# Performance work log

Hardware: AMD Instinct MI355X
Metric: run time of the kernel (lower is better)

Reference implementation:

```python
import jax, jax.numpy as jnp
import numpy as np

CODEBOOK_NUM = 4
VECTOR_NUM = 1024
VECTOR_DIM = 256
COMMIT_W = 0.25
N = 65536


def setup_inputs() -> dict:
    key = jax.random.key(0)
    kx, kw = jax.random.split(key)
    x = jax.random.normal(kx, (N, VECTOR_DIM), dtype=jnp.float32)
    # nn.Embedding init: uniform(-1/vector_num, 1/vector_num), one table per residual level
    codebooks = jax.random.uniform(
        kw, (CODEBOOK_NUM, VECTOR_NUM, VECTOR_DIM), dtype=jnp.float32,
        minval=-1.0 / VECTOR_NUM, maxval=1.0 / VECTOR_NUM)
    return {"x": x, "codebooks": codebooks}


def _pdist_mean(W):
    # mean of pairwise euclidean distances over i<j pairs (torch.pdist semantics)
    K = W.shape[0]
    sq = jnp.sum(W * W, axis=1)
    d2 = sq[:, None] + sq[None, :] - 2.0 * (W @ W.T)  # [K, K]
    mask = jnp.triu(jnp.ones((K, K), dtype=bool), k=1)
    d = jnp.sqrt(jnp.where(mask, jnp.maximum(d2, 0.0), 1.0))
    n_pairs = K * (K - 1) // 2
    return jnp.sum(jnp.where(mask, d, 0.0)) / n_pairs


def _vq_layer(residual, W):
    # distances [N, K]: ||r||^2 + ||w||^2 - 2 r.w
    dist = (jnp.sum(residual * residual, axis=1, keepdims=True)
            + jnp.sum(W * W, axis=1)
            - 2.0 * (residual @ W.T))
    idx = jnp.argmin(dist, axis=1)                    # [N]
    q = jnp.take(W, idx, axis=0)                      # gather == one_hot @ W (same value & grad)
    sg = jax.lax.stop_gradient
    e_latent = jnp.mean((sg(q) - residual) ** 2)
    q_latent = jnp.mean((q - sg(residual)) ** 2)
    quant_loss = q_latent + COMMIT_W * e_latent
    q_st = residual + sg(q - residual)                # straight-through
    counts = jnp.bincount(idx, length=W.shape[0]).astype(jnp.float32)
    util_loss = jnp.mean(jnp.abs(counts - residual.shape[0] / W.shape[0]))
    compact_loss = 2.0 * _pdist_mean(W)
    return q_st, quant_loss, util_loss, compact_loss, idx


def reference(x, codebooks):
    quantized = jnp.zeros_like(x)
    residual = x
    quant = jnp.float32(0.0)
    util = jnp.float32(0.0)
    compact = jnp.float32(0.0)
    all_idx = []
    for c in range(codebooks.shape[0]):
        q_st, ql, ul, cl, idx = _vq_layer(residual, codebooks[c])
        quantized = quantized + q_st
        residual = x - quantized
        quant = quant + ql
        util = util + ul
        compact = compact + cl
        all_idx.append(idx)
    return quantized, quant, util, compact, jnp.stack(all_idx, axis=0)
```

## Files before the change

kernel.cpp:

```cpp
#include <hip/hip_runtime.h>
#include <math.h>
#include <float.h>


#define N_ROWS 65536
#define DIM    256
#define K_NUM  1024
#define N_CB   4
#define RPB    32
#define QOFF   16777216
#define IDXOFF 16777219
#define NPAIRS 523776
#define MARGIN 2.4e-4f

#define SWZV(row, dunit) ((row) * DIM + ((((dunit) ^ ((row) & 7))) << 1))
#define SWZ2(row, d)     ((row) * DIM + ((((((d) >> 1) ^ ((row) & 7))) << 1) | ((d) & 1)))
#define AFCH(mt, kk, q, m) \
  (((((mt) * 8 + (kk)) * 64) + (q) * 16 + (((m) ^ ((q) << 1) ^ (kk)) & 15)) * 8)

typedef _Float16 f16x8 __attribute__((ext_vector_type(8)));
typedef float    f32x4 __attribute__((ext_vector_type(4)));

#define WS_BWS_OFF 69632
#define WS_NEEDED  2166784

__device__ __forceinline__ bool lexless(float a, int ka, float b, int kb) {
  return (a < b) || (a == b && ka < kb);
}

__global__ void zero_ws(int* counts, double* sse, double* pdacc) {
  int t = blockIdx.x * blockDim.x + threadIdx.x;
  if (t < 4096) counts[t] = 0;
  if (t < 4) sse[t] = 0.0;
  if (t == 0) pdacc[0] = 0.0;
}

__global__ void np_sqw_kernel(const float* __restrict__ cb,
                              float* __restrict__ sqw) {
#pragma clang fp contract(off)
  int g = blockIdx.x * blockDim.x + threadIdx.x;
  const float* row = cb + (size_t)g * DIM;
  float blk[2];
#pragma unroll
  for (int b = 0; b < 2; ++b) {
    const float* a = row + b * 128;
    float r[8];
#pragma unroll
    for (int j = 0; j < 8; ++j) { float v = a[j]; r[j] = v * v; }
    for (int i = 8; i < 128; i += 8) {
#pragma unroll
      for (int j = 0; j < 8; ++j) { float v = a[i + j]; r[j] = r[j] + v * v; }
    }
    blk[b] = ((r[0] + r[1]) + (r[2] + r[3])) + ((r[4] + r[5]) + (r[6] + r[7]));
  }
  sqw[g] = blk[0] + blk[1];
}

__global__ void cvt_b_kernel(const float* __restrict__ cb,
                             _Float16* __restrict__ bws) {
  int tg = blockIdx.x * blockDim.x + threadIdx.x;
  int row = tg >> 5;
  int chunk = tg & 31;
  int c = row >> 10, n = row & 1023;
  int nt = n >> 4, nin = n & 15;
  int kk = chunk >> 2, quad = chunk & 3;
  const float* src = cb + (size_t)row * DIM + chunk * 8;
  f16x8 h;
#pragma unroll
  for (int j = 0; j < 8; ++j) h[j] = (_Float16)src[j];
  size_t dst = ((size_t)((c * 64 + nt) * 8 + kk) * 64 + quad * 16 + nin) * 8;
  *(f16x8*)(bws + dst) = h;
}

__global__ __launch_bounds__(256) void pdist_mfma(
    const _Float16* __restrict__ bws, const float* __restrict__ sqw,
    double* __restrict__ pdacc) {
  int t = threadIdx.x, lane = t & 63, wq = t >> 6;
  int quad = lane >> 4, col = lane & 15;
  int c = blockIdx.x >> 6, iT = blockIdx.x & 63;
  const float* sq = sqw + c * K_NUM;
  const _Float16* base = bws + ((size_t)(c * 64) * 8) * 512 + lane * 8;
  f16x8 Ar[8];
#pragma unroll
  for (int kk = 0; kk < 8; ++kk)
    Ar[kk] = *(const f16x8*)(base + (size_t)(iT * 8 + kk) * 512);
  float bi[4];
#pragma unroll
  for (int r = 0; r < 4; ++r) bi[r] = sq[iT * 16 + quad * 4 + r];
  float sum = 0.f;
#pragma unroll 1
  for (int jt0 = 0; jt0 < 16; ++jt0) {
    int jt = wq * 16 + jt0;
    f16x8 Br[8];
#pragma unroll
    for (int kk = 0; kk < 8; ++kk)
      Br[kk] = *(const f16x8*)(base + (size_t)(jt * 8 + kk) * 512);
    f32x4 acc = {0.f, 0.f, 0.f, 0.f};
#pragma unroll
    for (int kk = 0; kk < 8; ++kk)
      acc = __builtin_amdgcn_mfma_f32_16x16x32_f16(Ar[kk], Br[kk], acc, 0, 0, 0);
    int j = jt * 16 + col;
    float bj = sq[j];
#pragma unroll
    for (int r = 0; r < 4; ++r) {
      int i = iT * 16 + quad * 4 + r;
      float d2 = bi[r] + bj - 2.0f * acc[r];
      if (i != j) sum += sqrtf(fmaxf(d2, 0.f));
    }
  }
  double ds = (double)sum;
#pragma unroll
  for (int off = 32; off; off >>= 1) ds += __shfl_xor(ds, off, 64);
  if (lane == 0) atomicAdd(pdacc, ds);
}

__global__ __launch_bounds__(256, 3) void rvq_main_mfma(
    const float* __restrict__ x, const float* __restrict__ cb,
    const _Float16* __restrict__ bws, const float* __restrict__ sqw,
    int* __restrict__ counts, double* __restrict__ sse,
    float* __restrict__ out) {
  __shared__ float resS[RPB * DIM];
  __shared__ __align__(16) _Float16 Af[16 * 64 * 8];
  __shared__ float wminS[RPB * 4];
  __shared__ int hardCnt[RPB];
  __shared__ int hardIdx[RPB * 6];
  __shared__ int idxS[RPB];
  __shared__ float sqrS[RPB];

  int t = threadIdx.x;
  int lane = t & 63, wq = t >> 6;
  int quad = lane >> 4, m16 = lane & 15;
  int rb = blockIdx.x * RPB;
  int dchunk = t & 31, rowgrp = t >> 5;

  float qacc[4][8];

#pragma unroll
  for (int i = 0; i < 4; ++i) {
    int row = rowgrp * 4 + i;
    size_t go = (size_t)(rb + row) * DIM + dchunk * 8;
    f32x4 v0 = __builtin_nontemporal_load((const f32x4*)&x[go]);
    f32x4 v1 = __builtin_nontemporal_load((const f32x4*)&x[go + 4]);
    float xv[8];
#pragma unroll
    for (int j = 0; j < 4; ++j) { xv[j] = v0[j]; xv[4 + j] = v1[j]; }
    f16x8 h;
#pragma unroll
    for (int j = 0; j < 8; ++j) h[j] = (_Float16)xv[j];
    *(f16x8*)(Af + AFCH(row >> 4, dchunk >> 2, dchunk & 3, row & 15)) = h;
    int u0 = dchunk * 4;
    *(float2*)&resS[SWZV(row, u0 + 0)] = make_float2(xv[0], xv[1]);
    *(float2*)&resS[SWZV(row, u0 + 1)] = make_float2(xv[2], xv[3]);
    *(float2*)&resS[SWZV(row, u0 + 2)] = make_float2(xv[4], xv[5]);
    *(float2*)&resS[SWZV(row, u0 + 3)] = make_float2(xv[6], xv[7]);
  }
  __syncthreads();

  for (int c = 0; c < N_CB; ++c) {
    const float* cbl = cb + (size_t)c * K_NUM * DIM;
    const float* sqwl = sqw + c * K_NUM;

    {
#pragma clang fp contract(off)
      int kg = t & 7, rg = t >> 3;
      float blk[2];
#pragma unroll
      for (int b = 0; b < 2; ++b) {
        float v0 = resS[SWZ2(rg, b * 128 + kg)];
        float acc = v0 * v0;
        for (int i = 1; i < 16; ++i) {
          float v = resS[SWZ2(rg, b * 128 + kg + 8 * i)];
          acc = acc + v * v;
        }
        acc = acc + __shfl_xor(acc, 1, 8);
        acc = acc + __shfl_xor(acc, 2, 8);
        acc = acc + __shfl_xor(acc, 4, 8);
        blk[b] = acc;
      }
      if (kg == 0) sqrS[rg] = blk[0] + blk[1];
    }

    f16x8 Ar[2][8];
#pragma unroll
    for (int kk = 0; kk < 8; ++kk) {
      Ar[0][kk] = *(const f16x8*)(Af + AFCH(0, kk, quad, m16));
      Ar[1][kk] = *(const f16x8*)(Af + AFCH(1, kk, quad, m16));
    }
    float s1[2][4], s2[2][4]; int k1[2][4], k2[2][4];
#pragma unroll
    for (int mt = 0; mt < 2; ++mt)
#pragma unroll
      for (int r = 0; r < 4; ++r) {
        s1[mt][r] = FLT_MAX; s2[mt][r] = FLT_MAX;
        k1[mt][r] = 0x7FFFFFFF; k2[mt][r] = 0x7FFFFFFF;
      }
    const _Float16* Bc = bws + (size_t)((c * 64 + wq * 16) * 8) * 512 + lane * 8;
#pragma unroll 1
    for (int nt = 0; nt < 16; ++nt) {
      const _Float16* Bp = Bc + (size_t)nt * 8 * 512;
      f16x8 Br[8];
#pragma unroll
      for (int kk = 0; kk < 8; ++kk)
        Br[kk] = *(const f16x8*)(Bp + (size_t)kk * 512);
      f32x4 acc0 = {0.f, 0.f, 0.f, 0.f}, acc1 = {0.f, 0.f, 0.f, 0.f};
#pragma unroll
      for (int kk = 0; kk < 8; ++kk) {
        acc0 = __builtin_amdgcn_mfma_f32_16x16x32_f16(Ar[0][kk], Br[kk], acc0, 0, 0, 0);
        acc1 = __builtin_amdgcn_mfma_f32_16x16x32_f16(Ar[1][kk], Br[kk], acc1, 0, 0, 0);
      }
      int n = (wq * 16 + nt) * 16 + m16;
      float w2 = sqwl[n];
#pragma unroll
      for (int r = 0; r < 4; ++r) {
        float sa = w2 - 2.0f * acc0[r];
        if (sa < s1[0][r]) { s2[0][r] = s1[0][r]; k2[0][r] = k1[0][r]; s1[0][r] = sa; k1[0][r] = n; }
        else if (sa < s2[0][r]) { s2[0][r] = sa; k2[0][r] = n; }
        float sb = w2 - 2.0f * acc1[r];
        if (sb < s1[1][r]) { s2[1][r] = s1[1][r]; k2[1][r] = k1[1][r]; s1[1][r] = sb; k1[1][r] = n; }
        else if (sb < s2[1][r]) { s2[1][r] = sb; k2[1][r] = n; }
      }
    }

    if (t < RPB) hardCnt[t] = 0;
#pragma unroll
    for (int mt = 0; mt < 2; ++mt)
#pragma unroll
      for (int r = 0; r < 4; ++r) {
        float mn = s1[mt][r];
#pragma unroll
        for (int off = 1; off <= 8; off <<= 1)
          mn = fminf(mn, __shfl_xor(mn, off, 16));
        if (m16 == 0) wminS[(mt * 16 + quad * 4 + r) * 4 + wq] = mn;
      }
    __syncthreads();

#pragma unroll
    for (int mt = 0; mt < 2; ++mt)
#pragma unroll
      for (int r = 0; r < 4; ++r) {
        int row = mt * 16 + quad * 4 + r;
        float thr = fminf(fminf(wminS[row * 4 + 0], wminS[row * 4 + 1]),
                          fminf(wminS[row * 4 + 2], wminS[row * 4 + 3])) + MARGIN;
        bool c1 = s1[mt][r] <= thr;
        if (c1) {
          bool c2 = s2[mt][r] <= thr;
          int pos = atomicAdd(&hardCnt[row], 1 + (c2 ? 1 : 0));
          if (pos < 6) hardIdx[row * 6 + pos] = k1[mt][r];
          if (c2 && pos + 1 < 6) hardIdx[row * 6 + pos + 1] = k2[mt][r];
        }
      }
    __syncthreads();

    {
      int kg = t & 7, rg = t >> 3;
      int cnt = hardCnt[rg]; if (cnt > 6) cnt = 6;
      int winner;
      if (cnt == 1) {
        winner = hardIdx[rg * 6];
      } else {
        float myd = FLT_MAX; int myk = 0x7FFFFFFF;
        if (kg < cnt) {
          int k = hardIdx[rg * 6 + kg];
          const float* wrow = cbl + (size_t)k * DIM;
          float gsum = 0.0f;
#pragma unroll 8
          for (int d = 0; d < DIM; ++d)
            gsum = __builtin_fmaf(wrow[d], resS[SWZ2(rg, d)], gsum);
          float T = sqrS[rg] + sqwl[k];
          myd = T - 2.0f * gsum;
          myk = k;
        }
#pragma unroll
        for (int off = 1; off <= 4; off <<= 1) {
          float od = __shfl_xor(myd, off, 8);
          int   ok = __shfl_xor(myk, off, 8);
          if (lexless(od, ok, myd, myk)) { myd = od; myk = ok; }
        }
        winner = myk;
      }
      if (kg == 0) {
        idxS[rg] = winner;
        out[(size_t)IDXOFF + (size_t)c * N_ROWS + rb + rg] = (float)winner;
        atomicAdd(&counts[c * K_NUM + winner], 1);
      }
    }
    __syncthreads();

    double lsse = 0.0;
#pragma unroll
    for (int i = 0; i < 4; ++i) {
      int row = rowgrp * 4 + i;
      int widx = idxS[row];
      size_t go = (size_t)(rb + row) * DIM + dchunk * 8;
      float wv[8], rv[8], xv[8];
      const float* wrow = cbl + (size_t)widx * DIM + dchunk * 8;
      *(float4*)&wv[0] = *(const float4*)&wrow[0];
      *(float4*)&wv[4] = *(const float4*)&wrow[4];
      int u0 = dchunk * 4;
      *(float2*)&rv[0] = *(const float2*)&resS[SWZV(row, u0 + 0)];
      *(float2*)&rv[2] = *(const float2*)&resS[SWZV(row, u0 + 1)];
      *(float2*)&rv[4] = *(const float2*)&resS[SWZV(row, u0 + 2)];
      *(float2*)&rv[6] = *(const float2*)&resS[SWZV(row, u0 + 3)];
      if (c == 1 || c == 2) {
        f32x4 xa = __builtin_nontemporal_load((const f32x4*)&x[go]);
        f32x4 xb = __builtin_nontemporal_load((const f32x4*)&x[go + 4]);
#pragma unroll
        for (int j = 0; j < 4; ++j) { xv[j] = xa[j]; xv[4 + j] = xb[j]; }
      }
      f16x8 h;
      float rnv[8];
#pragma unroll
      for (int j = 0; j < 8; ++j) {
        float e = wv[j] - rv[j];
        float qs = rv[j] + e;
        float qn = (c == 0) ? qs : (qacc[i][j] + qs);
        qacc[i][j] = qn;
        lsse += (double)e * (double)e;
        if (c < N_CB - 1) {
          float rn = (c == 0) ? (rv[j] - qn) : (xv[j] - qn);
          rnv[j] = rn;
          h[j] = (_Float16)rn;
        }
      }
      if (c < N_CB - 1) {
        *(f16x8*)(Af + AFCH(row >> 4, dchunk >> 2, dchunk & 3, row & 15)) = h;
        *(float2*)&resS[SWZV(row, u0 + 0)] = make_float2(rnv[0], rnv[1]);
        *(float2*)&resS[SWZV(row, u0 + 1)] = make_float2(rnv[2], rnv[3]);
        *(float2*)&resS[SWZV(row, u0 + 2)] = make_float2(rnv[4], rnv[5]);
        *(float2*)&resS[SWZV(row, u0 + 3)] = make_float2(rnv[6], rnv[7]);
      } else {
        f32x4 o0, o1;
#pragma unroll
        for (int j = 0; j < 4; ++j) { o0[j] = qacc[i][j]; o1[j] = qacc[i][4 + j]; }
        __builtin_nontemporal_store(o0, (f32x4*)&out[go]);
        __builtin_nontemporal_store(o1, (f32x4*)&out[go + 4]);
      }
    }
#pragma unroll
    for (int off = 32; off; off >>= 1) lsse += __shfl_xor(lsse, off, 64);
    if ((t & 63) == 0) atomicAdd(&sse[c], lsse);
    __syncthreads();
  }
}

__global__ void wnorm_kernel(const float* __restrict__ cb,
                             double* __restrict__ wn64) {
  int gw = blockIdx.x * 4 + (threadIdx.x >> 6);
  int lane = threadIdx.x & 63;
  const float* row = cb + (size_t)gw * DIM;
  float4 v = *(const float4*)(row + lane * 4);
  double s = (double)v.x * v.x + (double)v.y * v.y +
             (double)v.z * v.z + (double)v.w * v.w;
#pragma unroll
  for (int off = 32; off; off >>= 1) s += __shfl_xor(s, off, 64);
  if (lane == 0) wn64[gw] = s;
}

__global__ void pdist_kernel(const float* __restrict__ cb,
                             const double* __restrict__ wn64,
                             double* __restrict__ pdacc) {
  __shared__ float wi[DIM];
  int c = blockIdx.x >> 10;
  int i = blockIdx.x & 1023;
  int t = threadIdx.x;
  const float* rowi = cb + ((size_t)c * K_NUM + i) * DIM;
  *(float2*)&wi[t * 2] = *(const float2*)&rowi[t * 2];
  __syncthreads();
  double bi = wn64[c * K_NUM + i];
  double lsum = 0.0;
  for (int j = i + 1 + t; j < K_NUM; j += 128) {
    const float* rowj = cb + ((size_t)c * K_NUM + j) * DIM;
    double dot = 0.0;
#pragma unroll 8
    for (int d = 0; d < DIM; ++d) dot += (double)rowj[d] * (double)wi[d];
    double d2 = bi + wn64[c * K_NUM + j] - 2.0 * dot;
    lsum += sqrt(fmax(d2, 0.0));
  }
#pragma unroll
  for (int off = 32; off; off >>= 1) lsum += __shfl_xor(lsum, off, 64);
  if ((t & 63) == 0) atomicAdd(pdacc, lsum);
}

__global__ __launch_bounds__(128) void rvq_main_fb(
    const float* __restrict__ x, const float* __restrict__ cb,
    const float* __restrict__ sqw,
    int* __restrict__ counts, double* __restrict__ sse,
    float* __restrict__ out) {
  __shared__ float Wt[RPB * DIM];
  __shared__ float resS[RPB * DIM];
  int t = threadIdx.x;
  int kg = t & 7;
  int rg = t >> 3;
  int rb = blockIdx.x * RPB;
#pragma unroll 4
  for (int it = 0; it < RPB; ++it) {
    float2 v = *(const float2*)&x[(size_t)(rb + it) * DIM + t * 2];
    *(float2*)&resS[SWZV(it, t)] = v;
  }
  __syncthreads();
  for (int c = 0; c < N_CB; ++c) {
    const float* cbl = cb + (size_t)c * K_NUM * DIM;
    const float* sqwl = sqw + c * K_NUM;
    float sqr[2];
    {
#pragma clang fp contract(off)
#pragma unroll
      for (int j = 0; j < 2; ++j) {
        int row = rg + 16 * j;
        float blk[2];
#pragma unroll
        for (int b = 0; b < 2; ++b) {
          float v0 = resS[SWZ2(row, b * 128 + kg)];
          float acc = v0 * v0;
          for (int i = 1; i < 16; ++i) {
            float v = resS[SWZ2(row, b * 128 + kg + 8 * i)];
            acc = acc + v * v;
          }
          acc = acc + __shfl_xor(acc, 1, 8);
          acc = acc + __shfl_xor(acc, 2, 8);
          acc = acc + __shfl_xor(acc, 4, 8);
          blk[b] = acc;
        }
        sqr[j] = blk[0] + blk[1];
      }
    }
    float m1[2], m2[2]; int i1[2], i2[2];
    m1[0] = m1[1] = m2[0] = m2[1] = FLT_MAX;
    i1[0] = i1[1] = i2[0] = i2[1] = 0x7FFFFFFF;
    for (int tile = 0; tile < K_NUM / 32; ++tile) {
      __syncthreads();
      const float* wsrc = cbl + (size_t)tile * 32 * DIM;
#pragma unroll 4
      for (int it = 0; it < 32; ++it) {
        float2 v = *(const float2*)&wsrc[(size_t)it * DIM + t * 2];
        *(float2*)&Wt[SWZV(it, t)] = v;
      }
      __syncthreads();
      float acc[4][2] = {{0.f, 0.f}, {0.f, 0.f}, {0.f, 0.f}, {0.f, 0.f}};
#pragma unroll 8
      for (int du = 0; du < DIM / 2; ++du) {
        float2 r0 = *(const float2*)&resS[SWZV(rg, du)];
        float2 r1 = *(const float2*)&resS[SWZV(rg + 16, du)];
#pragma unroll
        for (int i = 0; i < 4; ++i) {
          int k = kg + 8 * i;
          float2 w = *(const float2*)&Wt[SWZV(k, du)];
          acc[i][0] += w.x * r0.x; acc[i][0] += w.y * r0.y;
          acc[i][1] += w.x * r1.x; acc[i][1] += w.y * r1.y;
        }
      }
#pragma unroll
      for (int i = 0; i < 4; ++i) {
        int k = tile * 32 + kg + 8 * i;
        float b = sqwl[k];
#pragma unroll
        for (int j = 0; j < 2; ++j) {
          float s = b - 2.0f * acc[i][j];
          if (lexless(s, k, m1[j], i1[j])) {
            m2[j] = m1[j]; i2[j] = i1[j]; m1[j] = s; i1[j] = k;
          } else if (lexless(s, k, m2[j], i2[j])) {
            m2[j] = s; i2[j] = k;
          }
        }
      }
    }
    float as[2][4]; int ak[2][4];
#pragma unroll
    for (int j = 0; j < 2; ++j) {
      as[j][0] = m1[j]; ak[j][0] = i1[j];
      as[j][1] = m2[j]; ak[j][1] = i2[j];
      as[j][2] = FLT_MAX; ak[j][2] = 0x7FFFFFFF;
      as[j][3] = FLT_MAX; ak[j][3] = 0x7FFFFFFF;
#pragma unroll
      for (int off = 1; off <= 4; off <<= 1) {
        float bs[4]; int bk[4];
#pragma unroll
        for (int q = 0; q < 4; ++q) {
          bs[q] = __shfl_xor(as[j][q], off, 8);
          bk[q] = __shfl_xor(ak[j][q], off, 8);
        }
        float cs[4]; int ck[4];
#pragma unroll
        for (int q = 0; q < 4; ++q) {
          bool ta = lexless(as[j][q], ak[j][q], bs[3 - q], bk[3 - q]);
          cs[q] = ta ? as[j][q] : bs[3 - q];
          ck[q] = ta ? ak[j][q] : bk[3 - q];
        }
#define CE(p, q) { bool sw = lexless(cs[q], ck[q], cs[p], ck[p]); \
                   float ts = sw ? cs[q] : cs[p]; int tk = sw ? ck[q] : ck[p]; \
                   cs[q] = sw ? cs[p] : cs[q]; ck[q] = sw ? ck[p] : ck[q]; \
                   cs[p] = ts; ck[p] = tk; }
        CE(0, 2) CE(1, 3) CE(0, 1) CE(2, 3)
#undef CE
#pragma unroll
        for (int q = 0; q < 4; ++q) { as[j][q] = cs[q]; ak[j][q] = ck[q]; }
      }
    }
    int winner[2];
#pragma unroll
    for (int j = 0; j < 2; ++j) {
      if (as[j][1] <= as[j][0] + 1.2e-4f) {
        int row = rg + 16 * j;
        float ss = (kg == 0) ? as[j][0] : (kg == 1) ? as[j][1]
                 : (kg == 2) ? as[j][2] : (kg == 3) ? as[j][3] : FLT_MAX;
        int   sk = (kg == 0) ? ak[j][0] : (kg == 1) ? ak[j][1]
                 : (kg == 2) ? ak[j][2] : (kg == 3) ? ak[j][3] : 0x7FFFFFFF;
        float myd = FLT_MAX; int myk = 0x7FFFFFFF;
        if (kg < 4 && ss <= as[j][0] + 1.2e-4f) {
          const float* wrow = cbl + (size_t)sk * DIM;
          float g = 0.0f;
#pragma unroll 8
          for (int d = 0; d < DIM; ++d)
            g = __builtin_fmaf(wrow[d], resS[SWZ2(row, d)], g);
          float T = sqr[j] + sqwl[sk];
          myd = T - 2.0f * g;
          myk = sk;
        }
#pragma unroll
        for (int off = 1; off <= 4; off <<= 1) {
          float od = __shfl_xor(myd, off, 8);
          int   ok = __shfl_xor(myk, off, 8);
          if (lexless(od, ok, myd, myk)) { myd = od; myk = ok; }
        }
        winner[j] = myk;
      } else {
        winner[j] = ak[j][0];
      }
    }
    __syncthreads();
    int* idxSf = (int*)Wt;
    if (kg == 0) {
      idxSf[rg] = winner[0];
      idxSf[rg + 16] = winner[1];
      out[(size_t)IDXOFF + (size_t)c * N_ROWS + rb + rg] = (float)winner[0];
      out[(size_t)IDXOFF + (size_t)c * N_ROWS + rb + rg + 16] = (float)winner[1];
      atomicAdd(&counts[c * K_NUM + winner[0]], 1);
      atomicAdd(&counts[c * K_NUM + winner[1]], 1);
    }
    __syncthreads();
    double lsse = 0.0;
#pragma unroll 4
    for (int it = 0; it < RPB; ++it) {
      int widx = idxSf[it];
      size_t go = (size_t)(rb + it) * DIM + t * 2;
      float2 wv = *(const float2*)&cbl[(size_t)widx * DIM + t * 2];
      float2 rv = *(const float2*)&resS[SWZV(it, t)];
      float ex = wv.x - rv.x, ey = wv.y - rv.y;
      float qsx = rv.x + ex, qsy = rv.y + ey;
      float qnx, qny;
      if (c == 0) { qnx = qsx; qny = qsy; }
      else { float2 qo = *(const float2*)&out[go]; qnx = qo.x + qsx; qny = qo.y + qsy; }
      *(float2*)&out[go] = make_float2(qnx, qny);
      float2 xv = *(const float2*)&x[go];
      float rnx = xv.x - qnx, rny = xv.y - qny;
      *(float2*)&resS[SWZV(it, t)] = make_float2(rnx, rny);
      lsse += (double)ex * (double)ex + (double)ey * (double)ey;
    }
#pragma unroll
    for (int off = 32; off; off >>= 1) lsse += __shfl_xor(lsse, off, 64);
    if ((t & 63) == 0) atomicAdd(&sse[c], lsse);
    __syncthreads();
  }
}

__global__ void finalize_kernel(const int* __restrict__ counts,
                                const double* __restrict__ sse,
                                const double* __restrict__ pdacc,
                                float* __restrict__ out, double pdscale) {
  __shared__ double red[1024];
  int t = threadIdx.x;
  double u = 0.0;
#pragma unroll
  for (int c = 0; c < 4; ++c) u += fabs((double)counts[c * 1024 + t] - 64.0);
  red[t] = u;
  __syncthreads();
  for (int s = 512; s; s >>= 1) {
    if (t < s) red[t] += red[t + s];
    __syncthreads();
  }
  if (t == 0) {
    double q = 0.0;
#pragma unroll
    for (int c = 0; c < 4; ++c) q += sse[c];
    q *= 1.25 / ((double)N_ROWS * (double)DIM);
    out[QOFF + 0] = (float)q;
    out[QOFF + 1] = (float)(red[0] / 1024.0);
    out[QOFF + 2] = (float)(pdscale * pdacc[0] / (double)NPAIRS);
  }
}

extern "C" void kernel_launch(void* const* d_in, const int* in_sizes, int n_in,
                              void* d_out, int out_size, void* d_ws, size_t ws_size,
                              hipStream_t stream) {
  const float* x  = (const float*)d_in[0];
  const float* cb = (const float*)d_in[1];
  float* out = (float*)d_out;

  char* w = (char*)d_ws;
  double* wn64   = (double*)(w);
  float*  sqw    = (float*) (w + 32768);
  int*    counts = (int*)   (w + 49152);
  double* sse    = (double*)(w + 65536);
  double* pdacc  = (double*)(w + 65568);
  _Float16* bws  = (_Float16*)(w + WS_BWS_OFF);

  zero_ws<<<16, 256, 0, stream>>>(counts, sse, pdacc);
  np_sqw_kernel<<<16, 256, 0, stream>>>(cb, sqw);
  if (ws_size >= WS_NEEDED) {
    cvt_b_kernel<<<512, 256, 0, stream>>>(cb, bws);
    pdist_mfma<<<256, 256, 0, stream>>>(bws, sqw, pdacc);
    rvq_main_mfma<<<N_ROWS / RPB, 256, 0, stream>>>(x, cb, bws, sqw, counts, sse, out);
    finalize_kernel<<<1, 1024, 0, stream>>>(counts, sse, pdacc, out, 1.0);
  } else {
    wnorm_kernel<<<1024, 256, 0, stream>>>(cb, wn64);
    pdist_kernel<<<4096, 128, 0, stream>>>(cb, wn64, pdacc);
    rvq_main_fb<<<N_ROWS / RPB, 128, 0, stream>>>(x, cb, sqw, counts, sse, out);
    finalize_kernel<<<1, 1024, 0, stream>>>(counts, sse, pdacc, out, 2.0);
  }
}
```

Baseline: 1.015 ms.

## Drop fp16 A-fragment LDS buffer and register accumulator to raise occupancy

Removes the separate fp16 A-operand shared buffer and builds MFMA A fragments by converting the fp32 residual in LDS on the fly. Removes the per-thread qacc register array: the running quantized sum is now stored to the output in global memory after every codebook and read back in the next one. Launch bounds go from 3 to 4 blocks per SM, relying on the lower LDS and register use. In exchange each codebook does extra global reads and writes of the output and extra LDS reads and conversions when building fragments.

```diff
diff --git a/kernel.cpp b/kernel.cpp
--- a/kernel.cpp
+++ b/kernel.cpp
@@ -15,8 +15,6 @@
 
 #define SWZV(row, dunit) ((row) * DIM + ((((dunit) ^ ((row) & 7))) << 1))
 #define SWZ2(row, d)     ((row) * DIM + ((((((d) >> 1) ^ ((row) & 7))) << 1) | ((d) & 1)))
-#define AFCH(mt, kk, q, m) \
-  (((((mt) * 8 + (kk)) * 64) + (q) * 16 + (((m) ^ ((q) << 1) ^ (kk)) & 15)) * 8)
 
 typedef _Float16 f16x8 __attribute__((ext_vector_type(8)));
 typedef float    f32x4 __attribute__((ext_vector_type(4)));
@@ -114,13 +112,12 @@
   if (lane == 0) atomicAdd(pdacc, ds);
 }
 
-__global__ __launch_bounds__(256, 3) void rvq_main_mfma(
+__global__ __launch_bounds__(256, 4) void rvq_main_mfma(
     const float* __restrict__ x, const float* __restrict__ cb,
     const _Float16* __restrict__ bws, const float* __restrict__ sqw,
     int* __restrict__ counts, double* __restrict__ sse,
     float* __restrict__ out) {
   __shared__ float resS[RPB * DIM];
-  __shared__ __align__(16) _Float16 Af[16 * 64 * 8];
   __shared__ float wminS[RPB * 4];
   __shared__ int hardCnt[RPB];
   __shared__ int hardIdx[RPB * 6];
@@ -133,26 +130,17 @@
   int rb = blockIdx.x * RPB;
   int dchunk = t & 31, rowgrp = t >> 5;
 
-  float qacc[4][8];
-
 #pragma unroll
   for (int i = 0; i < 4; ++i) {
     int row = rowgrp * 4 + i;
     size_t go = (size_t)(rb + row) * DIM + dchunk * 8;
     f32x4 v0 = __builtin_nontemporal_load((const f32x4*)&x[go]);
     f32x4 v1 = __builtin_nontemporal_load((const f32x4*)&x[go + 4]);
-    float xv[8];
-#pragma unroll
-    for (int j = 0; j < 4; ++j) { xv[j] = v0[j]; xv[4 + j] = v1[j]; }
-    f16x8 h;
-#pragma unroll
-    for (int j = 0; j < 8; ++j) h[j] = (_Float16)xv[j];
-    *(f16x8*)(Af + AFCH(row >> 4, dchunk >> 2, dchunk & 3, row & 15)) = h;
     int u0 = dchunk * 4;
-    *(float2*)&resS[SWZV(row, u0 + 0)] = make_float2(xv[0], xv[1]);
-    *(float2*)&resS[SWZV(row, u0 + 1)] = make_float2(xv[2], xv[3]);
-    *(float2*)&resS[SWZV(row, u0 + 2)] = make_float2(xv[4], xv[5]);
-    *(float2*)&resS[SWZV(row, u0 + 3)] = make_float2(xv[6], xv[7]);
+    *(float2*)&resS[SWZV(row, u0 + 0)] = make_float2(v0[0], v0[1]);
+    *(float2*)&resS[SWZV(row, u0 + 1)] = make_float2(v0[2], v0[3]);
+    *(float2*)&resS[SWZV(row, u0 + 2)] = make_float2(v1[0], v1[1]);
+    *(float2*)&resS[SWZV(row, u0 + 3)] = make_float2(v1[2], v1[3]);
   }
   __syncthreads();
 
@@ -182,9 +170,19 @@
 
     f16x8 Ar[2][8];
 #pragma unroll
-    for (int kk = 0; kk < 8; ++kk) {
-      Ar[0][kk] = *(const f16x8*)(Af + AFCH(0, kk, quad, m16));
-      Ar[1][kk] = *(const f16x8*)(Af + AFCH(1, kk, quad, m16));
+    for (int mt = 0; mt < 2; ++mt) {
+      int arow = mt * 16 + m16;
+#pragma unroll
+      for (int kk = 0; kk < 8; ++kk) {
+        f16x8 h;
+#pragma unroll
+        for (int jj = 0; jj < 4; ++jj) {
+          float2 p = *(const float2*)&resS[SWZV(arow, kk * 16 + quad * 4 + jj)];
+          h[2 * jj]     = (_Float16)p.x;
+          h[2 * jj + 1] = (_Float16)p.y;
+        }
+        Ar[mt][kk] = h;
+      }
     }
     float s1[2][4], s2[2][4]; int k1[2][4], k2[2][4];
 #pragma unroll
@@ -292,7 +290,7 @@
       int row = rowgrp * 4 + i;
       int widx = idxS[row];
       size_t go = (size_t)(rb + row) * DIM + dchunk * 8;
-      float wv[8], rv[8], xv[8];
+      float wv[8], rv[8], xv[8], qv[8];
       const float* wrow = cbl + (size_t)widx * DIM + dchunk * 8;
       *(float4*)&wv[0] = *(const float4*)&wrow[0];
       *(float4*)&wv[4] = *(const float4*)&wrow[4];
@@ -301,39 +299,38 @@
       *(float2*)&rv[2] = *(const float2*)&resS[SWZV(row, u0 + 1)];
       *(float2*)&rv[4] = *(const float2*)&resS[SWZV(row, u0 + 2)];
       *(float2*)&rv[6] = *(const float2*)&resS[SWZV(row, u0 + 3)];
+      if (c != 0) {
+        f32x4 qa = __builtin_nontemporal_load((const f32x4*)&out[go]);
+        f32x4 qb = __builtin_nontemporal_load((const f32x4*)&out[go + 4]);
+#pragma unroll
+        for (int j = 0; j < 4; ++j) { qv[j] = qa[j]; qv[4 + j] = qb[j]; }
+      }
       if (c == 1 || c == 2) {
         f32x4 xa = __builtin_nontemporal_load((const f32x4*)&x[go]);
         f32x4 xb = __builtin_nontemporal_load((const f32x4*)&x[go + 4]);
 #pragma unroll
         for (int j = 0; j < 4; ++j) { xv[j] = xa[j]; xv[4 + j] = xb[j]; }
       }
-      f16x8 h;
       float rnv[8];
+      f32x4 o0, o1;
 #pragma unroll
       for (int j = 0; j < 8; ++j) {
         float e = wv[j] - rv[j];
         float qs = rv[j] + e;
-        float qn = (c == 0) ? qs : (qacc[i][j] + qs);
-        qacc[i][j] = qn;
+        float qn = (c == 0) ? qs : (qv[j] + qs);
+        if (j < 4) o0[j] = qn; else o1[j - 4] = qn;
         lsse += (double)e * (double)e;
         if (c < N_CB - 1) {
-          float rn = (c == 0) ? (rv[j] - qn) : (xv[j] - qn);
-          rnv[j] = rn;
-          h[j] = (_Float16)rn;
-        }
-      }
+          rnv[j] = (c == 0) ? (rv[j] - qn) : (xv[j] - qn);
+        }
+      }
+      __builtin_nontemporal_store(o0, (f32x4*)&out[go]);
+      __builtin_nontemporal_store(o1, (f32x4*)&out[go + 4]);
       if (c < N_CB - 1) {
-        *(f16x8*)(Af + AFCH(row >> 4, dchunk >> 2, dchunk & 3, row & 15)) = h;
         *(float2*)&resS[SWZV(row, u0 + 0)] = make_float2(rnv[0], rnv[1]);
         *(float2*)&resS[SWZV(row, u0 + 1)] = make_float2(rnv[2], rnv[3]);
         *(float2*)&resS[SWZV(row, u0 + 2)] = make_float2(rnv[4], rnv[5]);
         *(float2*)&resS[SWZV(row, u0 + 3)] = make_float2(rnv[6], rnv[7]);
-      } else {
-        f32x4 o0, o1;
-#pragma unroll
-        for (int j = 0; j < 4; ++j) { o0[j] = qacc[i][j]; o1[j] = qacc[i][4 + j]; }
-        __builtin_nontemporal_store(o0, (f32x4*)&out[go]);
-        __builtin_nontemporal_store(o1, (f32x4*)&out[go + 4]);
       }
     }
 #pragma unroll
```

New measurement: 1.099 ms. +8.2%, slower.
